# Optimization experiments

Hardware: AMD Instinct MI355X
Metric: run time of the kernel (lower is better)

Reference implementation:

```python
import jax, jax.numpy as jnp
import numpy as np

B, T, H, OUT = 2048, 256, 512, 1


def setup_inputs() -> dict:
    key = jax.random.key(0)
    ks = jax.random.split(key, 11)
    s = 1.0 / np.sqrt(H)
    return {
        "x": jax.random.normal(ks[0], (B, T), dtype=jnp.float32),
        # weights stored as (in, out), i.e. torch Linear weight transposed
        "Wx0": jax.random.normal(ks[1], (1, H), dtype=jnp.float32) * s,
        "bx0": jax.random.normal(ks[2], (H,), dtype=jnp.float32) * s,
        "Wh0": jax.random.normal(ks[3], (H, H), dtype=jnp.float32) * s,
        "bh0": jax.random.normal(ks[4], (H,), dtype=jnp.float32) * s,
        "Wx1": jax.random.normal(ks[5], (H, H), dtype=jnp.float32) * s,
        "bx1": jax.random.normal(ks[6], (H,), dtype=jnp.float32) * s,
        "Wh1": jax.random.normal(ks[7], (H, H), dtype=jnp.float32) * s,
        "bh1": jax.random.normal(ks[8], (H,), dtype=jnp.float32) * s,
        "Wfc": jax.random.normal(ks[9], (H, OUT), dtype=jnp.float32) * s,
        "bfc": jax.random.normal(ks[10], (OUT,), dtype=jnp.float32) * s,
    }


def reference(x, Wx0, bx0, Wh0, bh0, Wx1, bx1, Wh1, bh1, Wfc, bfc):
    # Stacked 2-layer Elman RNN: h_l[t] = tanh(W_in_l @ in + b_in_l + W_h_l @ h_l[t-1] + b_h_l)
    batch = x.shape[0]
    hdim = Wh0.shape[0]
    h0 = jnp.zeros((batch, hdim), dtype=x.dtype)
    h1 = jnp.zeros((batch, hdim), dtype=x.dtype)

    def step(carry, xt):
        h0, h1 = carry
        # layer 0: scalar input per timestep -> outer product with Wx0 row
        h0 = jnp.tanh(xt[:, None] * Wx0[0] + bx0 + h0 @ Wh0 + bh0)
        # layer 1 consumes the NEW h0 (matches the in-place loop in torch)
        h1 = jnp.tanh(h0 @ Wx1 + bx1 + h1 @ Wh1 + bh1)
        return (h0, h1), None

    (h0, h1), _ = jax.lax.scan(step, (h0, h1), x.T)  # scan over time [T, B]
    return h1 @ Wfc + bfc  # [B, OUT]
```

## Files before the change

### kernel.cpp

```cpp
#include <hip/hip_runtime.h>
#include <hip/hip_bf16.h>


typedef _Float16 half8 __attribute__((ext_vector_type(8)));
typedef float f32x4 __attribute__((ext_vector_type(4)));

#define T_STEPS 256
#define H_DIM   512
#define BM      16

#define AS1 __attribute__((address_space(1)))
#define AS3 __attribute__((address_space(3)))

#define VMW4 asm volatile("s_waitcnt vmcnt(4)" ::: "memory")
#define VMW0 asm volatile("s_waitcnt vmcnt(0)" ::: "memory")
#define BARRIER() do { \
    asm volatile("s_waitcnt lgkmcnt(0)" ::: "memory"); \
    __builtin_amdgcn_s_barrier(); \
    asm volatile("" ::: "memory"); \
  } while (0)

__device__ __forceinline__ float tanh_fast(float z){
  float az = fabsf(z);
  float e  = __expf(-2.0f * az);
  float r  = (1.0f - e) * __builtin_amdgcn_rcpf(1.0f + e);
  return copysignf(r, z);
}

__global__ void prep_w_45028437131357(const float* __restrict__ W,
                                      half8* __restrict__ out){
  int tid  = blockIdx.x * 256 + threadIdx.x;
  int lane = tid & 63;
  int kc   = (tid >> 6) & 15;
  int nt   = tid >> 10;
  int col  = nt * 16 + (lane & 15);
  int k0   = kc * 32 + (lane >> 4) * 8;
  half8 v;
#pragma unroll
  for (int j = 0; j < 8; ++j) v[j] = (_Float16)W[(k0 + j) * H_DIM + col];
  out[tid] = v;
}

__device__ __forceinline__ void stage4(const half8* M, int kc, char* dstBase,
                                       int w4, int lane){
#pragma unroll
  for (int i = 0; i < 4; ++i)
    __builtin_amdgcn_global_load_lds(
        (const AS1 void*)(M + ((w4 + i) * 16 + kc) * 64 + lane),
        (AS3 void*)(dstBase + i * 1024), 16, 0, 0);
}

__device__ __forceinline__ void stage_gn(int gn, const half8* W0,
                                         const half8* W1, const half8* WX,
                                         char* Sw, int w4, int lane){
  const half8* M = (gn < 16) ? W0 : ((gn < 32) ? W1 : WX);
  stage4(M, gn & 15, Sw + ((gn & 1) << 15), w4, lane);
}


__global__ __launch_bounds__(512, 2)
void rnn_main_45028437131357(const float* __restrict__ x,
                             const float* __restrict__ Wx0,
                             const float* __restrict__ bx0,
                             const float* __restrict__ bh0,
                             const float* __restrict__ bx1,
                             const float* __restrict__ bh1,
                             const float* __restrict__ Wfc,
                             const float* __restrict__ bfc,
                             const half8* __restrict__ Wh0f,
                             const half8* __restrict__ Wx1f,
                             const half8* __restrict__ Wh1f,
                             float* __restrict__ out){
  __shared__ __align__(16) char  h0s[BM * 1024];
  __shared__ __align__(16) char  h1s[BM * 1024];
  __shared__ __align__(16) char  Ss[2 * 8 * 4096];
  __shared__ float xls[16];

  const int tid  = threadIdx.x;
  const int lane = tid & 63;
  const int w    = tid >> 6;
  const int w4   = 4 * w;
  const int r0   = blockIdx.x * BM;
  char* Sw = Ss + w * 4096;

  for (int i = tid; i < BM * 256; i += 512){
    ((float*)h0s)[i] = 0.0f;
    ((float*)h1s)[i] = 0.0f;
  }

  const int cl      = lane & 15;
  const int kg      = lane >> 4;
  const int aBase   = cl * 1024 + kg * 16;
  const int aSwz    = (cl & 7) << 4;
  const int rowBase = kg * 4;

  float wx0c[4], b0c[4], b1c[4];
  int   colA[4];
#pragma unroll
  for (int i = 0; i < 4; ++i){
    int col = (w4 + i) * 16 + cl;
    colA[i] = col;
    wx0c[i] = Wx0[col];
    b0c[i]  = bx0[col] + bh0[col];
    b1c[i]  = bx1[col] + bh1[col];
  }

  float xreg = (tid < BM) ? x[(r0 + tid) * T_STEPS] : 0.0f;

  stage_gn(0, Wh0f, Wh1f, Wx1f, Sw, w4, lane);

  const f32x4 z4 = {0.f, 0.f, 0.f, 0.f};

  for (int t = 0; t < T_STEPS; ++t){
    if (tid < BM) xls[tid] = xreg;
    BARRIER();
    {
      int tn = (t + 1 < T_STEPS) ? t + 1 : t;
      if (tid < BM) xreg = x[(r0 + tid) * T_STEPS + tn];
    }

    f32x4 acc0[4] = {z4, z4, z4, z4};
    f32x4 acc1[4] = {z4, z4, z4, z4};

#define CONSUME(APTR, ACC)                                                     \
    {                                                                          \
      const char* sb = Sw + ((kc & 1) << 15);                                  \
      half8 a   = *(const half8*)((APTR) + ((aBase + kc * 64) ^ aSwz));        \
      half8 bb0 = *(const half8*)(sb +    0 + lane * 16);                      \
      half8 bb1 = *(const half8*)(sb + 1024 + lane * 16);                      \
      half8 bb2 = *(const half8*)(sb + 2048 + lane * 16);                      \
      half8 bb3 = *(const half8*)(sb + 3072 + lane * 16);                      \
      ACC[0] = __builtin_amdgcn_mfma_f32_16x16x32_f16(a, bb0, ACC[0], 0,0,0);  \
      ACC[1] = __builtin_amdgcn_mfma_f32_16x16x32_f16(a, bb1, ACC[1], 0,0,0);  \
      ACC[2] = __builtin_amdgcn_mfma_f32_16x16x32_f16(a, bb2, ACC[2], 0,0,0);  \
      ACC[3] = __builtin_amdgcn_mfma_f32_16x16x32_f16(a, bb3, ACC[3], 0,0,0);  \
    }

    for (int kc = 0; kc < 16; ++kc){
      stage_gn(kc + 1, Wh0f, Wh1f, Wx1f, Sw, w4, lane);
      VMW4;
      CONSUME(h0s, acc0);
    }
    for (int kc = 0; kc < 16; ++kc){
      stage_gn(17 + kc, Wh0f, Wh1f, Wx1f, Sw, w4, lane);
      VMW4;
      CONSUME(h1s, acc1);
    }

    _Float16 nh0[4][4];
    {
      float xv[4];
#pragma unroll
      for (int rg = 0; rg < 4; ++rg) xv[rg] = xls[rowBase + rg];
#pragma unroll
      for (int i = 0; i < 4; ++i)
#pragma unroll
        for (int rg = 0; rg < 4; ++rg)
          nh0[i][rg] = (_Float16)tanh_fast(acc0[i][rg] + b0c[i] + xv[rg] * wx0c[i]);
    }
    BARRIER();
#pragma unroll
    for (int i = 0; i < 4; ++i)
#pragma unroll
      for (int rg = 0; rg < 4; ++rg){
        int row = rowBase + rg;
        *(_Float16*)(h0s + row * 1024 +
                     ((colA[i] * 2) ^ ((row & 7) << 4))) = nh0[i][rg];
      }
    BARRIER();

    for (int kc = 0; kc < 16; ++kc){
      int gnext = 33 + kc;
      if (gnext < 48){
        stage_gn(gnext, Wh0f, Wh1f, Wx1f, Sw, w4, lane);
        VMW4;
      } else if (t + 1 < T_STEPS){
        stage_gn(0, Wh0f, Wh1f, Wx1f, Sw, w4, lane);
        VMW4;
      } else {
        VMW0;
      }
      CONSUME(h0s, acc1);
    }

#pragma unroll
    for (int i = 0; i < 4; ++i)
#pragma unroll
      for (int rg = 0; rg < 4; ++rg){
        int row = rowBase + rg;
        *(_Float16*)(h1s + row * 1024 +
                     ((colA[i] * 2) ^ ((row & 7) << 4))) =
            (_Float16)tanh_fast(acc1[i][rg] + b1c[i]);
      }
#undef CONSUME
  }
  BARRIER();

  {
    int r  = tid >> 5;
    int g2 = tid & 31;
    float p = 0.0f;
#pragma unroll
    for (int k2 = 0; k2 < 16; ++k2){
      int c = g2 + 32 * k2;
      float hv = (float)*(const _Float16*)(h1s + r * 1024 +
                                           ((c * 2) ^ ((r & 7) << 4)));
      p += hv * Wfc[c];
    }
#pragma unroll
    for (int off = 16; off >= 1; off >>= 1) p += __shfl_xor(p, off);
    if (g2 == 0) out[r0 + r] = p + bfc[0];
  }
}

extern "C" void kernel_launch(void* const* d_in, const int* in_sizes, int n_in,
                              void* d_out, int out_size, void* d_ws, size_t ws_size,
                              hipStream_t stream) {
  const float* x   = (const float*)d_in[0];
  const float* Wx0 = (const float*)d_in[1];
  const float* bx0 = (const float*)d_in[2];
  const float* Wh0 = (const float*)d_in[3];
  const float* bh0 = (const float*)d_in[4];
  const float* Wx1 = (const float*)d_in[5];
  const float* bx1 = (const float*)d_in[6];
  const float* Wh1 = (const float*)d_in[7];
  const float* bh1 = (const float*)d_in[8];
  const float* Wfc = (const float*)d_in[9];
  const float* bfc = (const float*)d_in[10];

  _Float16* wsH = (_Float16*)d_ws;
  half8* Wh0f = (half8*)(wsH);
  half8* Wx1f = (half8*)(wsH + 262144);
  half8* Wh1f = (half8*)(wsH + 524288);

  prep_w_45028437131357<<<128, 256, 0, stream>>>(Wh0, Wh0f);
  prep_w_45028437131357<<<128, 256, 0, stream>>>(Wx1, Wx1f);
  prep_w_45028437131357<<<128, 256, 0, stream>>>(Wh1, Wh1f);

  rnn_main_45028437131357<<<128, 512, 0, stream>>>(
      x, Wx0, bx0, bh0, bx1, bh1, Wfc, bfc,
      (const half8*)Wh0f, (const half8*)Wx1f, (const half8*)Wh1f,
      (float*)d_out);
}
```

Baseline: 13.28 ms.

## Triple-buffer weight staging with deeper prefetch, stagger K order, preload x into LDS

Weight chunks now use a per-wave triple buffer in LDS. Each chunk is issued two steps ahead, with the wait relaxed from vmcnt(4) to vmcnt(8), to hide more global/L2 latency behind the MFMA work. Each group of blocks starts its K loop at a different offset (koff) so concurrent blocks hit different weight chunks, and the inner loops are fully unrolled. All of x for the block's rows is loaded once into swizzled LDS, replacing the per-step global load and broadcast. The cost is more LDS (larger staging area plus the x tile) and larger unrolled code with higher register pressure.

After: 12.32 ms, median of 4. 1.08x faster.

```diff
diff --git a/kernel.cpp b/kernel.cpp
--- a/kernel.cpp
+++ b/kernel.cpp
@@ -12,7 +12,7 @@
 #define AS1 __attribute__((address_space(1)))
 #define AS3 __attribute__((address_space(3)))
 
-#define VMW4 asm volatile("s_waitcnt vmcnt(4)" ::: "memory")
+#define VMW8 asm volatile("s_waitcnt vmcnt(8)" ::: "memory")
 #define VMW0 asm volatile("s_waitcnt vmcnt(0)" ::: "memory")
 #define BARRIER() do { \
     asm volatile("s_waitcnt lgkmcnt(0)" ::: "memory"); \
@@ -41,20 +41,18 @@
   out[tid] = v;
 }
 
-__device__ __forceinline__ void stage4(const half8* M, int kc, char* dstBase,
-                                       int w4, int lane){
+__device__ __forceinline__ void stage_g(int g, int koff, const half8* W0,
+                                        const half8* W1, const half8* WX,
+                                        char* Sw, int w4, int lane){
+  int g48 = (g >= 48) ? g - 48 : g;
+  const half8* M = (g48 < 16) ? W0 : ((g48 < 32) ? W1 : WX);
+  int keff = ((g48 & 15) + koff) & 15;
+  char* dst = Sw + (g % 3) * 4096;
 #pragma unroll
   for (int i = 0; i < 4; ++i)
     __builtin_amdgcn_global_load_lds(
-        (const AS1 void*)(M + ((w4 + i) * 16 + kc) * 64 + lane),
-        (AS3 void*)(dstBase + i * 1024), 16, 0, 0);
-}
-
-__device__ __forceinline__ void stage_gn(int gn, const half8* W0,
-                                         const half8* W1, const half8* WX,
-                                         char* Sw, int w4, int lane){
-  const half8* M = (gn < 16) ? W0 : ((gn < 32) ? W1 : WX);
-  stage4(M, gn & 15, Sw + ((gn & 1) << 15), w4, lane);
+        (const AS1 void*)(M + ((w4 + i) * 16 + keff) * 64 + lane),
+        (AS3 void*)(dst + i * 1024), 16, 0, 0);
 }
 
 
@@ -73,19 +71,22 @@
                              float* __restrict__ out){
   __shared__ __align__(16) char  h0s[BM * 1024];
   __shared__ __align__(16) char  h1s[BM * 1024];
-  __shared__ __align__(16) char  Ss[2 * 8 * 4096];
-  __shared__ float xls[16];
+  __shared__ __align__(16) float xall[BM * 256];
+  __shared__ __align__(16) char  Ss[8 * 3 * 4096];
 
   const int tid  = threadIdx.x;
   const int lane = tid & 63;
   const int w    = tid >> 6;
   const int w4   = 4 * w;
   const int r0   = blockIdx.x * BM;
-  char* Sw = Ss + w * 4096;
+  const int koff = (blockIdx.x >> 3) & 15;
+  char* Sw = Ss + w * 12288;
 
   for (int i = tid; i < BM * 256; i += 512){
     ((float*)h0s)[i] = 0.0f;
     ((float*)h1s)[i] = 0.0f;
+    int r = i >> 8, c = i & 255;
+    xall[r * 256 + (c ^ ((r & 7) << 2))] = x[(r0 + r) * T_STEPS + c];
   }
 
   const int cl      = lane & 15;
@@ -105,53 +106,53 @@
     b1c[i]  = bx1[col] + bh1[col];
   }
 
-  float xreg = (tid < BM) ? x[(r0 + tid) * T_STEPS] : 0.0f;
-
-  stage_gn(0, Wh0f, Wh1f, Wx1f, Sw, w4, lane);
+  stage_g(0, koff, Wh0f, Wh1f, Wx1f, Sw, w4, lane);
+  stage_g(1, koff, Wh0f, Wh1f, Wx1f, Sw, w4, lane);
 
   const f32x4 z4 = {0.f, 0.f, 0.f, 0.f};
 
+#define CONSUME(APTR, ACC, KC, G)                                             \
+    {                                                                         \
+      int keff = ((KC) + koff) & 15;                                          \
+      const char* sb = Sw + ((G) % 3) * 4096;                                 \
+      half8 a   = *(const half8*)((APTR) + ((aBase + keff * 64) ^ aSwz));     \
+      half8 bb0 = *(const half8*)(sb +    0 + lane * 16);                     \
+      half8 bb1 = *(const half8*)(sb + 1024 + lane * 16);                     \
+      half8 bb2 = *(const half8*)(sb + 2048 + lane * 16);                     \
+      half8 bb3 = *(const half8*)(sb + 3072 + lane * 16);                     \
+      ACC[0] = __builtin_amdgcn_mfma_f32_16x16x32_f16(a, bb0, ACC[0], 0,0,0); \
+      ACC[1] = __builtin_amdgcn_mfma_f32_16x16x32_f16(a, bb1, ACC[1], 0,0,0); \
+      ACC[2] = __builtin_amdgcn_mfma_f32_16x16x32_f16(a, bb2, ACC[2], 0,0,0); \
+      ACC[3] = __builtin_amdgcn_mfma_f32_16x16x32_f16(a, bb3, ACC[3], 0,0,0); \
+    }
+
   for (int t = 0; t < T_STEPS; ++t){
-    if (tid < BM) xls[tid] = xreg;
     BARRIER();
-    {
-      int tn = (t + 1 < T_STEPS) ? t + 1 : t;
-      if (tid < BM) xreg = x[(r0 + tid) * T_STEPS + tn];
-    }
 
     f32x4 acc0[4] = {z4, z4, z4, z4};
     f32x4 acc1[4] = {z4, z4, z4, z4};
 
-#define CONSUME(APTR, ACC)                                                     \
-    {                                                                          \
-      const char* sb = Sw + ((kc & 1) << 15);                                  \
-      half8 a   = *(const half8*)((APTR) + ((aBase + kc * 64) ^ aSwz));        \
-      half8 bb0 = *(const half8*)(sb +    0 + lane * 16);                      \
-      half8 bb1 = *(const half8*)(sb + 1024 + lane * 16);                      \
-      half8 bb2 = *(const half8*)(sb + 2048 + lane * 16);                      \
-      half8 bb3 = *(const half8*)(sb + 3072 + lane * 16);                      \
-      ACC[0] = __builtin_amdgcn_mfma_f32_16x16x32_f16(a, bb0, ACC[0], 0,0,0);  \
-      ACC[1] = __builtin_amdgcn_mfma_f32_16x16x32_f16(a, bb1, ACC[1], 0,0,0);  \
-      ACC[2] = __builtin_amdgcn_mfma_f32_16x16x32_f16(a, bb2, ACC[2], 0,0,0);  \
-      ACC[3] = __builtin_amdgcn_mfma_f32_16x16x32_f16(a, bb3, ACC[3], 0,0,0);  \
-    }
-
+#pragma unroll
     for (int kc = 0; kc < 16; ++kc){
-      stage_gn(kc + 1, Wh0f, Wh1f, Wx1f, Sw, w4, lane);
-      VMW4;
-      CONSUME(h0s, acc0);
-    }
+      stage_g(kc + 2, koff, Wh0f, Wh1f, Wx1f, Sw, w4, lane);
+      VMW8;
+      CONSUME(h0s, acc0, kc, kc);
+    }
+#pragma unroll
     for (int kc = 0; kc < 16; ++kc){
-      stage_gn(17 + kc, Wh0f, Wh1f, Wx1f, Sw, w4, lane);
-      VMW4;
-      CONSUME(h1s, acc1);
+      stage_g(18 + kc, koff, Wh0f, Wh1f, Wx1f, Sw, w4, lane);
+      VMW8;
+      CONSUME(h1s, acc1, kc, 16 + kc);
     }
 
     _Float16 nh0[4][4];
     {
       float xv[4];
 #pragma unroll
-      for (int rg = 0; rg < 4; ++rg) xv[rg] = xls[rowBase + rg];
+      for (int rg = 0; rg < 4; ++rg){
+        int row = rowBase + rg;
+        xv[rg] = xall[row * 256 + (t ^ ((row & 7) << 2))];
+      }
 #pragma unroll
       for (int i = 0; i < 4; ++i)
 #pragma unroll
@@ -169,18 +170,11 @@
       }
     BARRIER();
 
+#pragma unroll
     for (int kc = 0; kc < 16; ++kc){
-      int gnext = 33 + kc;
-      if (gnext < 48){
-        stage_gn(gnext, Wh0f, Wh1f, Wx1f, Sw, w4, lane);
-        VMW4;
-      } else if (t + 1 < T_STEPS){
-        stage_gn(0, Wh0f, Wh1f, Wx1f, Sw, w4, lane);
-        VMW4;
-      } else {
-        VMW0;
-      }
-      CONSUME(h0s, acc1);
+      stage_g(34 + kc, koff, Wh0f, Wh1f, Wx1f, Sw, w4, lane);
+      VMW8;
+      CONSUME(h0s, acc1, kc, 32 + kc);
     }
 
 #pragma unroll
@@ -192,8 +186,9 @@
                      ((colA[i] * 2) ^ ((row & 7) << 4))) =
             (_Float16)tanh_fast(acc1[i][rg] + b1c[i]);
       }
+  }
 #undef CONSUME
-  }
+  VMW0;
   BARRIER();
 
   {
```
